# Kernel tuning notes

Measured on AMD Instinct MI355X. Metric: run time of the kernel, lower is better.

The kernel has to match this reference:

```python
import jax, jax.numpy as jnp
import numpy as np

B, S, D, H, L, DFF = 16, 256, 768, 12, 6, 2048
IMG, P, C = 256, 16, 3
HD = D // H
EPS = 1e-5


def _n(k, shp, scale=0.02):
    return jax.random.normal(k, shp, jnp.float32) * scale


def setup_inputs() -> dict:
    key = jax.random.key(0)
    ks = jax.random.split(key, 9)
    return dict(
        encoded_patches=jax.random.normal(ks[0], (B, S, D), jnp.float32),
        W_self_in=_n(ks[1], (L, 3 * D, D)), b_self_in=jnp.zeros((L, 3 * D), jnp.float32),
        W_self_out=_n(ks[2], (L, D, D)), b_self_out=jnp.zeros((L, D), jnp.float32),
        W_cross_in=_n(ks[3], (L, 3 * D, D)), b_cross_in=jnp.zeros((L, 3 * D), jnp.float32),
        W_cross_out=_n(ks[4], (L, D, D)), b_cross_out=jnp.zeros((L, D), jnp.float32),
        ln1_g=jnp.ones((L, D), jnp.float32), ln1_b=jnp.zeros((L, D), jnp.float32),
        ln2_g=jnp.ones((L, D), jnp.float32), ln2_b=jnp.zeros((L, D), jnp.float32),
        ln3_g=jnp.ones((L, D), jnp.float32), ln3_b=jnp.zeros((L, D), jnp.float32),
        W_ff1=_n(ks[5], (L, DFF, D)), b_ff1=jnp.zeros((L, DFF), jnp.float32),
        W_ff2=_n(ks[6], (L, D, DFF)), b_ff2=jnp.zeros((L, D), jnp.float32),
        W_patch=_n(ks[7], (C * P * P, D)), b_patch=jnp.zeros((C * P * P,), jnp.float32),
    )


def sinusoidal_pe(seq, d):
    pos = jnp.arange(seq, dtype=jnp.float32)[:, None]
    div = jnp.exp(jnp.arange(0, d, 2, dtype=jnp.float32) * (-np.log(10000.0) / d))
    pe = jnp.zeros((seq, d), jnp.float32)
    pe = pe.at[:, 0::2].set(jnp.sin(pos * div))
    pe = pe.at[:, 1::2].set(jnp.cos(pos * div))
    return pe


def layer_norm(x, g, b):
    mu = x.mean(-1, keepdims=True)
    var = ((x - mu) ** 2).mean(-1, keepdims=True)
    return (x - mu) * jax.lax.rsqrt(var + EPS) * g + b


def mha(q_in, kv_in, W_in, b_in, W_out, b_out, mask):
    # W_in: [3D, D] packed q,k,v (PyTorch in_proj layout); Linear: y = x W^T + b
    Wq, Wk, Wv = jnp.split(W_in, 3, axis=0)
    bq, bk, bv = jnp.split(b_in, 3, axis=0)
    Bq = q_in.shape[0]
    q = (q_in @ Wq.T + bq).reshape(Bq, -1, H, HD)
    k = (kv_in @ Wk.T + bk).reshape(Bq, -1, H, HD)
    v = (kv_in @ Wv.T + bv).reshape(Bq, -1, H, HD)
    scores = jnp.einsum('bqhd,bkhd->bhqk', q, k) / np.sqrt(HD)
    if mask is not None:
        scores = scores + mask  # mask broadcasts [S, S] with -inf above diag
    attn = jax.nn.softmax(scores, axis=-1)
    out = jnp.einsum('bhqk,bkhd->bqhd', attn, v).reshape(Bq, -1, D)
    return out @ W_out.T + b_out


def reference(encoded_patches, W_self_in, b_self_in, W_self_out, b_self_out,
              W_cross_in, b_cross_in, W_cross_out, b_cross_out,
              ln1_g, ln1_b, ln2_g, ln2_b, ln3_g, ln3_b,
              W_ff1, b_ff1, W_ff2, b_ff2, W_patch, b_patch):
    # The original loops over growing prefixes i=1..S and takes the last
    # position each time. With a causal self-attn mask and per-position
    # cross-attn/FFN/LN, that is mathematically identical to one full
    # causal pass; we compute it once. (eval mode: dropout = identity)
    pe = sinusoidal_pe(S, D)
    causal = jnp.where(jnp.triu(jnp.ones((S, S), jnp.float32), 1) > 0, -jnp.inf, 0.0)
    mem = encoded_patches
    x = encoded_patches + pe[None, :, :]
    for l in range(L):
        # post-norm TransformerDecoderLayer (PyTorch default norm_first=False)
        x = layer_norm(x + mha(x, x, W_self_in[l], b_self_in[l],
                               W_self_out[l], b_self_out[l], causal),
                       ln1_g[l], ln1_b[l])
        x = layer_norm(x + mha(x, mem, W_cross_in[l], b_cross_in[l],
                               W_cross_out[l], b_cross_out[l], None),
                       ln2_g[l], ln2_b[l])
        ff = jax.nn.relu(x @ W_ff1[l].T + b_ff1[l]) @ W_ff2[l].T + b_ff2[l]
        x = layer_norm(x + ff, ln3_g[l], ln3_b[l])
    out = x @ W_patch.T + b_patch                       # [B, S, C*P*P]
    out = out.reshape(-1, IMG, IMG, C)                  # naive view, as in source
    return jnp.transpose(out, (0, 3, 1, 2))             # [B, C, IMG, IMG]
```

## Files before the change

kernel.cpp:

```cpp
#include <hip/hip_runtime.h>
#include <hip/hip_bf16.h>

#define DEV __device__ __forceinline__

typedef __bf16 bf16x8 __attribute__((ext_vector_type(8)));
typedef __bf16 bf16x4 __attribute__((ext_vector_type(4)));
typedef float  f32x4  __attribute__((ext_vector_type(4)));

DEV bf16x8 cvt8(const float4 a, const float4 b) {
    bf16x8 r;
    r[0] = (__bf16)a.x; r[1] = (__bf16)a.y; r[2] = (__bf16)a.z; r[3] = (__bf16)a.w;
    r[4] = (__bf16)b.x; r[5] = (__bf16)b.y; r[6] = (__bf16)b.z; r[7] = (__bf16)b.w;
    return r;
}

DEV void gload_lds16(const __bf16* g, __bf16* l) {
    __builtin_amdgcn_global_load_lds(
        (const __attribute__((address_space(1))) void*)g,
        (__attribute__((address_space(3))) void*)l, 16, 0, 0);
}

DEV int swzcol(int col, int row) {
    return (col & ~63) | ((((col >> 3) & 7) ^ (row & 7)) << 3) | (col & 7);
}

DEV void wconv_one(const float* __restrict__ src, __bf16* __restrict__ dst,
                   int lg, int gpr, int K) {
    const int n = lg / gpr;
    const int gi = lg - n * gpr;
    const int cb = (gi >> 3) << 6;
    const int g = gi & 7;
    const float* sp = src + (size_t)n * K + cb + ((g ^ (n & 7)) << 3);
    float4 a = *(const float4*)sp;
    float4 b = *(const float4*)(sp + 4);
    *(bf16x8*)&dst[(size_t)lg * 8] = cvt8(a, b);
}

__global__ __launch_bounds__(256) void wconv(const float* __restrict__ W,
                                             __bf16* __restrict__ Wb) {
    const int gid = blockIdx.x * 256 + threadIdx.x;
    wconv_one(W, Wb, gid, 96, 768);
}

__global__ __launch_bounds__(256) void wconv4(const float* __restrict__ s0,
                                              const float* __restrict__ s1,
                                              const float* __restrict__ s2,
                                              const float* __restrict__ s3,
                                              __bf16* __restrict__ dst) {
    const int gid = blockIdx.x * 256 + threadIdx.x;
    if (gid < 221184)      wconv_one(s0, dst,           gid,          96, 768);
    else if (gid < 294912) wconv_one(s1, dst + 1769472, gid - 221184, 96, 768);
    else if (gid < 516096) wconv_one(s2, dst + 2359296, gid - 294912, 96, 768);
    else                   wconv_one(s3, dst + 4128768, gid - 516096, 96, 768);
}

__global__ __launch_bounds__(256) void wconv_ff(const float* __restrict__ f1,
                                                const float* __restrict__ f2,
                                                __bf16* __restrict__ dst) {
    const int gid = blockIdx.x * 256 + threadIdx.x;
    if (gid < 196608) wconv_one(f1, dst,           gid,          96, 768);
    else              wconv_one(f2, dst + 1572864, gid - 196608, 256, 2048);
}

template <int RELU, int OUT, int BN>
__global__ __launch_bounds__(256) void gemm_bt(const __bf16* __restrict__ Xb,
                                               const __bf16* __restrict__ Wb,
                                               const float* __restrict__ bias,
                                               float* __restrict__ Yf,
                                               __bf16* __restrict__ Yb,
                                               int ldy, int K) {
    __shared__ __bf16 As[128 * 64];
    __shared__ __bf16 Bs[BN * 64];

    const int tid = threadIdx.x;
    const int lane = tid & 63;
    const int wave = tid >> 6;
    constexpr int NI = (BN == 128) ? 4 : 2;
    const int wr = (BN == 128) ? (wave >> 1) : wave;
    const int wc = (BN == 128) ? (wave & 1) : 0;
    const int lr = lane & 15;

    const int nx = gridDim.x;
    int bid = blockIdx.y * nx + blockIdx.x;
    const int cpx = (nx * gridDim.y) >> 3;
    bid = (bid & 7) * cpx + (bid >> 3);
    const int by = bid / nx;
    const int bx = bid - by * nx;
    const int mBase = by * 128;
    const int nBase = bx * BN;

    const int brow = lane >> 3;
    const __bf16* Ap = Xb + (size_t)mBase * K + ((lane & 7) << 3);
    const __bf16* Bp = Wb + (size_t)nBase * K + ((lane & 7) << 3);

    f32x4 acc[NI][4];
#pragma unroll
    for (int i = 0; i < NI; ++i)
#pragma unroll
        for (int j = 0; j < 4; ++j) {
            f32x4 z = {0.f, 0.f, 0.f, 0.f};
            acc[i][j] = z;
        }

    for (int kt = 0; kt < K; kt += 64) {
#pragma unroll
        for (int i = 0; i < 4; ++i) {
            const int r0 = (wave << 5) + (i << 3);
            gload_lds16(Ap + (size_t)(r0 + brow) * K + kt, &As[r0 << 6]);
        }
#pragma unroll
        for (int i = 0; i < BN / 32; ++i) {
            const int r0 = wave * (BN / 4) + (i << 3);
            gload_lds16(Bp + (size_t)(r0 + brow) * K + kt, &Bs[r0 << 6]);
        }
        __syncthreads();
#pragma unroll
        for (int kk = 0; kk < 2; ++kk) {
            const int q = (lane >> 4) + (kk << 2);
            bf16x8 af[NI], bfv[4];
#pragma unroll
            for (int i = 0; i < NI; ++i) {
                const int r = wr * (NI * 16) + i * 16 + lr;
                af[i] = *(const bf16x8*)&As[(r << 6) + ((q ^ (r & 7)) << 3)];
            }
#pragma unroll
            for (int j = 0; j < 4; ++j) {
                const int r = wc * 64 + j * 16 + lr;
                bfv[j] = *(const bf16x8*)&Bs[(r << 6) + ((q ^ (r & 7)) << 3)];
            }
#pragma unroll
            for (int i = 0; i < NI; ++i)
#pragma unroll
                for (int j = 0; j < 4; ++j)
                    acc[i][j] = __builtin_amdgcn_mfma_f32_16x16x32_bf16(af[i], bfv[j], acc[i][j], 0, 0, 0);
        }
        __syncthreads();
    }

    const int rsub = (lane >> 4) << 2;
#pragma unroll
    for (int i = 0; i < NI; ++i)
#pragma unroll
        for (int j = 0; j < 4; ++j) {
            const int col = nBase + wc * 64 + j * 16 + lr;
            const float bv = bias[col];
#pragma unroll
            for (int rr = 0; rr < 4; ++rr) {
                const int row = mBase + wr * (NI * 16) + i * 16 + rsub + rr;
                float v = acc[i][j][rr] + bv;
                if (RELU) v = fmaxf(v, 0.f);
                if (OUT == 1) {
                    Yb[(size_t)row * ldy + swzcol(col, row)] = (__bf16)v;
                } else if (OUT == 2) {
                    const int b_ = row >> 8, s_ = row & 255;
                    const int w_ = col / 3, c_ = col - w_ * 3;
                    Yf[(size_t)b_ * 196608 + (size_t)c_ * 65536 + s_ * 256 + w_] = v;
                } else {
                    Yf[(size_t)row * ldy + col] = v;
                }
            }
        }
}

__global__ __launch_bounds__(256) void attn_mfma(const __bf16* __restrict__ QKV,
                                                 __bf16* __restrict__ Oout,
                                                 int causal) {
    const int bh = blockIdx.x;
    const int qq = blockIdx.y;
    const int b = bh / 12, h = bh - b * 12;
    const int tid = threadIdx.x;
    const int lane = tid & 63;
    const int w = tid >> 6;
    const int g = lane >> 4;
    const int c = lane & 15;
    const int c7 = c & 7;

    __shared__ __bf16 Ks[64 * 64];
    __shared__ __bf16 Vs[64 * 66];

    const int q64 = (w << 4) + c;
    const int qrow = (qq << 6) + q64;
    const __bf16* qp = QKV + (size_t)((b << 8) + qrow) * 2304 + (h << 6);
    bf16x8 qf0 = *(const bf16x8*)(qp + ((g ^ c7) << 3));
    bf16x8 qf1 = *(const bf16x8*)(qp + (((g + 4) ^ c7) << 3));

    f32x4 oacc[4];
#pragma unroll
    for (int i = 0; i < 4; ++i) { f32x4 z = {0.f, 0.f, 0.f, 0.f}; oacc[i] = z; }
    float mrun = -1e30f, lrun = 0.f;

    const int nt = causal ? (qq + 1) : 4;
    const int sr = tid >> 2;
    const int sg0 = (tid & 3) << 1;
    const int sp = sg0 << 3;

    for (int kt = 0; kt < nt; ++kt) {
        __syncthreads();
        {
            const __bf16* Kp = QKV + (size_t)((b << 8) + (kt << 6)) * 2304 + 768 + (h << 6) + ((lane & 7) << 3);
#pragma unroll
            for (int i = 0; i < 2; ++i) {
                const int r0 = (w << 4) + (i << 3);
                gload_lds16(Kp + (size_t)(r0 + (lane >> 3)) * 2304, &Ks[r0 << 6]);
            }
        }
        {
            const __bf16* vp = QKV + (size_t)((b << 8) + (kt << 6) + sr) * 2304 + 1536 + (h << 6);
            bf16x8 v0 = *(const bf16x8*)(vp + sp);
            bf16x8 v1 = *(const bf16x8*)(vp + sp + 8);
            const int s7 = sr & 7;
            uint32_t* d0 = (uint32_t*)&Vs[sr * 66 + ((sg0 ^ s7) << 3)];
            uint32_t* d1 = (uint32_t*)&Vs[sr * 66 + (((sg0 + 1) ^ s7) << 3)];
            const uint32_t* u0 = (const uint32_t*)&v0;
            const uint32_t* u1 = (const uint32_t*)&v1;
            d0[0] = u0[0]; d0[1] = u0[1]; d0[2] = u0[2]; d0[3] = u0[3];
            d1[0] = u1[0]; d1[1] = u1[1]; d1[2] = u1[2]; d1[3] = u1[3];
        }
        __syncthreads();

        f32x4 sc[4];
#pragma unroll
        for (int mf = 0; mf < 4; ++mf) { f32x4 z = {0.f, 0.f, 0.f, 0.f}; sc[mf] = z; }
#pragma unroll
        for (int mf = 0; mf < 4; ++mf) {
            const int row = (mf << 4) + c;
            bf16x8 af0 = *(const bf16x8*)&Ks[(row << 6) + ((g ^ c7) << 3)];
            sc[mf] = __builtin_amdgcn_mfma_f32_16x16x32_bf16(af0, qf0, sc[mf], 0, 0, 0);
            bf16x8 af1 = *(const bf16x8*)&Ks[(row << 6) + (((g + 4) ^ c7) << 3)];
            sc[mf] = __builtin_amdgcn_mfma_f32_16x16x32_bf16(af1, qf1, sc[mf], 0, 0, 0);
        }

        const int diag = (causal && kt == qq);
        float tm = -1e30f;
#pragma unroll
        for (int mf = 0; mf < 4; ++mf)
#pragma unroll
            for (int r = 0; r < 4; ++r) {
                float v = sc[mf][r] * 0.125f;
                if (diag && ((mf << 4) + (g << 2) + r > q64)) v = -1e30f;
                sc[mf][r] = v;
                tm = fmaxf(tm, v);
            }
        tm = fmaxf(tm, __shfl_xor(tm, 16));
        tm = fmaxf(tm, __shfl_xor(tm, 32));
        const float mnew = fmaxf(mrun, tm);
        const float rs = __expf(mrun - mnew);
        mrun = mnew;
        lrun *= rs;
#pragma unroll
        for (int i = 0; i < 4; ++i) {
            oacc[i][0] *= rs; oacc[i][1] *= rs; oacc[i][2] *= rs; oacc[i][3] *= rs;
        }

        __shared__ __bf16 Ps[64 * 64];
#pragma unroll
        for (int mf = 0; mf < 4; ++mf) {
            const int kg = (mf << 1) + (g >> 1);
            const int e = (g & 1) << 2;
#pragma unroll
            for (int r = 0; r < 4; ++r) {
                float p = __expf(sc[mf][r] - mnew);
                lrun += p;
                Ps[(q64 << 6) + ((kg ^ c7) << 3) + e + r] = (__bf16)p;
            }
        }

#pragma unroll
        for (int kc = 0; kc < 2; ++kc) {
            bf16x8 pb = *(const bf16x8*)&Ps[(q64 << 6) + (((g + (kc << 2)) ^ c7) << 3)];
#pragma unroll
            for (int df = 0; df < 4; ++df) {
                bf16x8 av;
#pragma unroll
                for (int j = 0; j < 8; ++j)
                    av[j] = Vs[((g << 3) + j + (kc << 5)) * 66 + (df << 4) + c];
                oacc[df] = __builtin_amdgcn_mfma_f32_16x16x32_bf16(av, pb, oacc[df], 0, 0, 0);
            }
        }
    }

    lrun += __shfl_xor(lrun, 16);
    lrun += __shfl_xor(lrun, 32);
    const float inv = 1.f / lrun;
    __bf16* op = Oout + (size_t)((b << 8) + qrow) * 768 + (h << 6);
#pragma unroll
    for (int df = 0; df < 4; ++df) {
        bf16x4 ov;
        ov[0] = (__bf16)(oacc[df][0] * inv);
        ov[1] = (__bf16)(oacc[df][1] * inv);
        ov[2] = (__bf16)(oacc[df][2] * inv);
        ov[3] = (__bf16)(oacc[df][3] * inv);
        const int gran = (df << 1) + (g >> 1);
        *(bf16x4*)(op + ((gran ^ c7) << 3) + ((g & 1) << 2)) = ov;
    }
}

__global__ __launch_bounds__(256) void resid_ln(float* __restrict__ x,
                                                __bf16* __restrict__ xb,
                                                const float* __restrict__ r,
                                                const float* __restrict__ g,
                                                const float* __restrict__ b) {
    const int row = blockIdx.x, tid = threadIdx.x;
    float* xp = x + (size_t)row * 768;
    __bf16* xbp = xb + (size_t)row * 768;
    const float* rp = r + (size_t)row * 768;

    float v0 = xp[tid] + rp[tid];
    float v1 = xp[tid + 256] + rp[tid + 256];
    float v2 = xp[tid + 512] + rp[tid + 512];

    __shared__ float red[4];
    float s = v0 + v1 + v2;
#pragma unroll
    for (int off = 32; off > 0; off >>= 1) s += __shfl_down(s, off, 64);
    if ((tid & 63) == 0) red[tid >> 6] = s;
    __syncthreads();
    const float mean = (red[0] + red[1] + red[2] + red[3]) * (1.0f / 768.0f);
    __syncthreads();

    float d0 = v0 - mean, d1 = v1 - mean, d2 = v2 - mean;
    float q = d0 * d0 + d1 * d1 + d2 * d2;
#pragma unroll
    for (int off = 32; off > 0; off >>= 1) q += __shfl_down(q, off, 64);
    if ((tid & 63) == 0) red[tid >> 6] = q;
    __syncthreads();
    const float inv = rsqrtf((red[0] + red[1] + red[2] + red[3]) * (1.0f / 768.0f) + 1e-5f);

    const float o0 = d0 * inv * g[tid] + b[tid];
    const float o1 = d1 * inv * g[tid + 256] + b[tid + 256];
    const float o2 = d2 * inv * g[tid + 512] + b[tid + 512];
    xp[tid] = o0;       xbp[swzcol(tid, row)] = (__bf16)o0;
    xp[tid + 256] = o1; xbp[swzcol(tid + 256, row)] = (__bf16)o1;
    xp[tid + 512] = o2; xbp[swzcol(tid + 512, row)] = (__bf16)o2;
}

__global__ __launch_bounds__(256) void add_pe(const float* __restrict__ e,
                                              float* __restrict__ x,
                                              __bf16* __restrict__ xb,
                                              __bf16* __restrict__ encb) {
    const int gid = blockIdx.x * 256 + threadIdx.x;
    const int m = gid / 96;
    const int g8 = gid - m * 96;
    const int col0 = g8 << 3;
    const int s = m & 255;

    float4 e0 = *(const float4*)(e + (size_t)m * 768 + col0);
    float4 e1 = *(const float4*)(e + (size_t)m * 768 + col0 + 4);

    float pe[8];
#pragma unroll
    for (int p = 0; p < 4; ++p) {
        const int d = col0 + 2 * p;
        const float div = __expf((float)d * (-0.011992630693328381f));
        const float ang = (float)s * div;
        pe[2 * p] = __sinf(ang);
        pe[2 * p + 1] = __cosf(ang);
    }
    float4 v0, v1;
    v0.x = e0.x + pe[0]; v0.y = e0.y + pe[1]; v0.z = e0.z + pe[2]; v0.w = e0.w + pe[3];
    v1.x = e1.x + pe[4]; v1.y = e1.y + pe[5]; v1.z = e1.z + pe[6]; v1.w = e1.w + pe[7];

    *(float4*)(x + (size_t)m * 768 + col0) = v0;
    *(float4*)(x + (size_t)m * 768 + col0 + 4) = v1;

    const int scb = (col0 & ~63) | ((((g8 & 7) ^ (m & 7)) << 3));
    *(bf16x8*)&xb[(size_t)m * 768 + scb] = cvt8(v0, v1);
    *(bf16x8*)&encb[(size_t)m * 768 + scb] = cvt8(e0, e1);
}

extern "C" void kernel_launch(void* const* d_in, const int* in_sizes, int n_in,
                              void* d_out, int out_size, void* d_ws, size_t ws_size,
                              hipStream_t stream) {
    const float* enc         = (const float*)d_in[0];
    const float* W_self_in   = (const float*)d_in[1];
    const float* b_self_in   = (const float*)d_in[2];
    const float* W_self_out  = (const float*)d_in[3];
    const float* b_self_out  = (const float*)d_in[4];
    const float* W_cross_in  = (const float*)d_in[5];
    const float* b_cross_in  = (const float*)d_in[6];
    const float* W_cross_out = (const float*)d_in[7];
    const float* b_cross_out = (const float*)d_in[8];
    const float* ln1_g       = (const float*)d_in[9];
    const float* ln1_b       = (const float*)d_in[10];
    const float* ln2_g       = (const float*)d_in[11];
    const float* ln2_b       = (const float*)d_in[12];
    const float* ln3_g       = (const float*)d_in[13];
    const float* ln3_b       = (const float*)d_in[14];
    const float* W_ff1       = (const float*)d_in[15];
    const float* b_ff1       = (const float*)d_in[16];
    const float* W_ff2       = (const float*)d_in[17];
    const float* b_ff2       = (const float*)d_in[18];
    const float* W_patch     = (const float*)d_in[19];
    const float* b_patch     = (const float*)d_in[20];

    float* out = (float*)d_out;
    float* ws  = (float*)d_ws;

    float*  x       = ws;
    __bf16* xb      = (__bf16*)(ws + 3145728);
    __bf16* qkvb    = (__bf16*)(ws + 4718592);
    __bf16* attnout = (__bf16*)(ws + 9437184);
    float*  proj    = ws + 11010048;
    __bf16* encb    = (__bf16*)(ws + 14155776);
    __bf16* wbuf    = (__bf16*)(ws + 15728640);

    add_pe<<<1536, 256, 0, stream>>>(enc, x, xb, encb);

    for (int l = 0; l < 6; ++l) {
        const float* Wsi = W_self_in   + (size_t)l * 2304 * 768;
        const float* Wso = W_self_out  + (size_t)l * 768 * 768;
        const float* Wci = W_cross_in  + (size_t)l * 2304 * 768;
        const float* Wco = W_cross_out + (size_t)l * 768 * 768;
        const float* Wf1 = W_ff1       + (size_t)l * 2048 * 768;
        const float* Wf2 = W_ff2       + (size_t)l * 768 * 2048;

        wconv4<<<2304, 256, 0, stream>>>(Wsi, Wso, Wci, Wco, wbuf);

        gemm_bt<0, 1, 128><<<dim3(18, 32), 256, 0, stream>>>(xb, wbuf, b_self_in + l * 2304,
                                                             nullptr, qkvb, 2304, 768);
        attn_mfma<<<dim3(192, 4), 256, 0, stream>>>(qkvb, attnout, 1);
        gemm_bt<0, 0, 64><<<dim3(12, 32), 256, 0, stream>>>(attnout, wbuf + 1769472,
                                                            b_self_out + l * 768,
                                                            proj, nullptr, 768, 768);
        resid_ln<<<4096, 256, 0, stream>>>(x, xb, proj, ln1_g + l * 768, ln1_b + l * 768);

        gemm_bt<0, 1, 64><<<dim3(12, 32), 256, 0, stream>>>(xb, wbuf + 2359296,
                                                            b_cross_in + l * 2304,
                                                            nullptr, qkvb, 2304, 768);
        gemm_bt<0, 1, 128><<<dim3(12, 32), 256, 0, stream>>>(encb, wbuf + 2949120,
                                                             b_cross_in + l * 2304 + 768,
                                                             nullptr, qkvb + 768, 2304, 768);
        attn_mfma<<<dim3(192, 4), 256, 0, stream>>>(qkvb, attnout, 0);
        gemm_bt<0, 0, 64><<<dim3(12, 32), 256, 0, stream>>>(attnout, wbuf + 4128768,
                                                            b_cross_out + l * 768,
                                                            proj, nullptr, 768, 768);
        resid_ln<<<4096, 256, 0, stream>>>(x, xb, proj, ln2_g + l * 768, ln2_b + l * 768);

        wconv_ff<<<1536, 256, 0, stream>>>(Wf1, Wf2, wbuf);
        gemm_bt<1, 1, 128><<<dim3(16, 32), 256, 0, stream>>>(xb, wbuf, b_ff1 + l * 2048,
                                                             nullptr, qkvb, 2048, 768);
        gemm_bt<0, 0, 64><<<dim3(12, 32), 256, 0, stream>>>(qkvb, wbuf + 1572864,
                                                            b_ff2 + l * 768,
                                                            proj, nullptr, 768, 2048);
        resid_ln<<<4096, 256, 0, stream>>>(x, xb, proj, ln3_g + l * 768, ln3_b + l * 768);
    }

    wconv<<<288, 256, 0, stream>>>(W_patch, wbuf);
    gemm_bt<0, 2, 64><<<dim3(12, 32), 256, 0, stream>>>(xb, wbuf, b_patch,
                                                        out, nullptr, 768, 768);
}
```

Baseline: 1.450 ms.

## Double-buffer GEMM LDS loads and emit bf16 projection outputs for residual LN

The GEMM main loop now keeps two LDS buffers. It issues the next k-tile's global-to-LDS loads before computing on the current one, using a partial vmcnt wait and raw barriers in place of full __syncthreads, so loads overlap MFMA work. Separately, the output-projection and FF2 GEMMs write bf16 instead of fp32, and resid_ln reads bf16 residuals, which halves that intermediate traffic. The cost is twice the LDS per block, which may lower occupancy, and extra rounding of the residual branch to bf16.

Result: faster. 1.352 ms (-6.7%).

```diff
diff --git a/kernel.cpp b/kernel.cpp
--- a/kernel.cpp
+++ b/kernel.cpp
@@ -2,6 +2,7 @@
 #include <hip/hip_bf16.h>
 
 #define DEV __device__ __forceinline__
+#define WAITVM(N) asm volatile("s_waitcnt vmcnt(" #N ")" ::: "memory")
 
 typedef __bf16 bf16x8 __attribute__((ext_vector_type(8)));
 typedef __bf16 bf16x4 __attribute__((ext_vector_type(4)));
@@ -69,8 +70,10 @@
                                                float* __restrict__ Yf,
                                                __bf16* __restrict__ Yb,
                                                int ldy, int K) {
-    __shared__ __bf16 As[128 * 64];
-    __shared__ __bf16 Bs[BN * 64];
+    constexpr int ABUF = 128 * 64;
+    constexpr int BBUF = BN * 64;
+    __shared__ __bf16 As[2 * ABUF];
+    __shared__ __bf16 Bs[2 * BBUF];
 
     const int tid = threadIdx.x;
     const int lane = tid & 63;
@@ -102,18 +105,20 @@
             acc[i][j] = z;
         }
 
-    for (int kt = 0; kt < K; kt += 64) {
+    auto STAGE = [&](int sel, int kt) {
 #pragma unroll
         for (int i = 0; i < 4; ++i) {
             const int r0 = (wave << 5) + (i << 3);
-            gload_lds16(Ap + (size_t)(r0 + brow) * K + kt, &As[r0 << 6]);
+            gload_lds16(Ap + (size_t)(r0 + brow) * K + kt, &As[sel * ABUF + (r0 << 6)]);
         }
 #pragma unroll
         for (int i = 0; i < BN / 32; ++i) {
             const int r0 = wave * (BN / 4) + (i << 3);
-            gload_lds16(Bp + (size_t)(r0 + brow) * K + kt, &Bs[r0 << 6]);
-        }
-        __syncthreads();
+            gload_lds16(Bp + (size_t)(r0 + brow) * K + kt, &Bs[sel * BBUF + (r0 << 6)]);
+        }
+    };
+
+    auto COMPUTE = [&](int sel) {
 #pragma unroll
         for (int kk = 0; kk < 2; ++kk) {
             const int q = (lane >> 4) + (kk << 2);
@@ -121,12 +126,12 @@
 #pragma unroll
             for (int i = 0; i < NI; ++i) {
                 const int r = wr * (NI * 16) + i * 16 + lr;
-                af[i] = *(const bf16x8*)&As[(r << 6) + ((q ^ (r & 7)) << 3)];
+                af[i] = *(const bf16x8*)&As[sel * ABUF + (r << 6) + ((q ^ (r & 7)) << 3)];
             }
 #pragma unroll
             for (int j = 0; j < 4; ++j) {
                 const int r = wc * 64 + j * 16 + lr;
-                bfv[j] = *(const bf16x8*)&Bs[(r << 6) + ((q ^ (r & 7)) << 3)];
+                bfv[j] = *(const bf16x8*)&Bs[sel * BBUF + (r << 6) + ((q ^ (r & 7)) << 3)];
             }
 #pragma unroll
             for (int i = 0; i < NI; ++i)
@@ -134,8 +139,24 @@
                 for (int j = 0; j < 4; ++j)
                     acc[i][j] = __builtin_amdgcn_mfma_f32_16x16x32_bf16(af[i], bfv[j], acc[i][j], 0, 0, 0);
         }
-        __syncthreads();
+    };
+
+    STAGE(0, 0);
+    int sel = 0;
+    for (int kt = 0; kt + 64 < K; kt += 64) {
+        STAGE(sel ^ 1, kt + 64);
+        if constexpr (BN == 128) WAITVM(8); else WAITVM(6);
+        __builtin_amdgcn_s_barrier();
+        __builtin_amdgcn_sched_barrier(0);
+        COMPUTE(sel);
+        __builtin_amdgcn_sched_barrier(0);
+        __builtin_amdgcn_s_barrier();
+        sel ^= 1;
     }
+    WAITVM(0);
+    __builtin_amdgcn_s_barrier();
+    __builtin_amdgcn_sched_barrier(0);
+    COMPUTE(sel);
 
     const int rsub = (lane >> 4) << 2;
 #pragma unroll
@@ -156,7 +177,7 @@
                     const int w_ = col / 3, c_ = col - w_ * 3;
                     Yf[(size_t)b_ * 196608 + (size_t)c_ * 65536 + s_ * 256 + w_] = v;
                 } else {
-                    Yf[(size_t)row * ldy + col] = v;
+                    Yb[(size_t)row * ldy + col] = (__bf16)v;
                 }
             }
         }
@@ -297,17 +318,17 @@
 
 __global__ __launch_bounds__(256) void resid_ln(float* __restrict__ x,
                                                 __bf16* __restrict__ xb,
-                                                const float* __restrict__ r,
+                                                const __bf16* __restrict__ r,
                                                 const float* __restrict__ g,
                                                 const float* __restrict__ b) {
     const int row = blockIdx.x, tid = threadIdx.x;
     float* xp = x + (size_t)row * 768;
     __bf16* xbp = xb + (size_t)row * 768;
-    const float* rp = r + (size_t)row * 768;
-
-    float v0 = xp[tid] + rp[tid];
-    float v1 = xp[tid + 256] + rp[tid + 256];
-    float v2 = xp[tid + 512] + rp[tid + 512];
+    const __bf16* rp = r + (size_t)row * 768;
+
+    float v0 = xp[tid] + (float)rp[tid];
+    float v1 = xp[tid + 256] + (float)rp[tid + 256];
+    float v2 = xp[tid + 512] + (float)rp[tid + 512];
 
     __shared__ float red[4];
     float s = v0 + v1 + v2;
@@ -400,7 +421,7 @@
     __bf16* xb      = (__bf16*)(ws + 3145728);
     __bf16* qkvb    = (__bf16*)(ws + 4718592);
     __bf16* attnout = (__bf16*)(ws + 9437184);
-    float*  proj    = ws + 11010048;
+    __bf16* projb   = (__bf16*)(ws + 11010048);
     __bf16* encb    = (__bf16*)(ws + 14155776);
     __bf16* wbuf    = (__bf16*)(ws + 15728640);
 
@@ -419,10 +440,10 @@
         gemm_bt<0, 1, 128><<<dim3(18, 32), 256, 0, stream>>>(xb, wbuf, b_self_in + l * 2304,
                                                              nullptr, qkvb, 2304, 768);
         attn_mfma<<<dim3(192, 4), 256, 0, stream>>>(qkvb, attnout, 1);
-        gemm_bt<0, 0, 64><<<dim3(12, 32), 256, 0, stream>>>(attnout, wbuf + 1769472,
+        gemm_bt<0, 3, 64><<<dim3(12, 32), 256, 0, stream>>>(attnout, wbuf + 1769472,
                                                             b_self_out + l * 768,
-                                                            proj, nullptr, 768, 768);
-        resid_ln<<<4096, 256, 0, stream>>>(x, xb, proj, ln1_g + l * 768, ln1_b + l * 768);
+                                                            nullptr, projb, 768, 768);
+        resid_ln<<<4096, 256, 0, stream>>>(x, xb, projb, ln1_g + l * 768, ln1_b + l * 768);
 
         gemm_bt<0, 1, 64><<<dim3(12, 32), 256, 0, stream>>>(xb, wbuf + 2359296,
                                                             b_cross_in + l * 2304,
@@ -431,18 +452,18 @@
                                                              b_cross_in + l * 2304 + 768,
                                                              nullptr, qkvb + 768, 2304, 768);
         attn_mfma<<<dim3(192, 4), 256, 0, stream>>>(qkvb, attnout, 0);
-        gemm_bt<0, 0, 64><<<dim3(12, 32), 256, 0, stream>>>(attnout, wbuf + 4128768,
+        gemm_bt<0, 3, 64><<<dim3(12, 32), 256, 0, stream>>>(attnout, wbuf + 4128768,
                                                             b_cross_out + l * 768,
-                                                            proj, nullptr, 768, 768);
-        resid_ln<<<4096, 256, 0, stream>>>(x, xb, proj, ln2_g + l * 768, ln2_b + l * 768);
+                                                            nullptr, projb, 768, 768);
+        resid_ln<<<4096, 256, 0, stream>>>(x, xb, projb, ln2_g + l * 768, ln2_b + l * 768);
 
         wconv_ff<<<1536, 256, 0, stream>>>(Wf1, Wf2, wbuf);
         gemm_bt<1, 1, 128><<<dim3(16, 32), 256, 0, stream>>>(xb, wbuf, b_ff1 + l * 2048,
                                                              nullptr, qkvb, 2048, 768);
-        gemm_bt<0, 0, 64><<<dim3(12, 32), 256, 0, stream>>>(qkvb, wbuf + 1572864,
+        gemm_bt<0, 3, 64><<<dim3(12, 32), 256, 0, stream>>>(qkvb, wbuf + 1572864,
                                                             b_ff2 + l * 768,
-                                                            proj, nullptr, 768, 2048);
-        resid_ln<<<4096, 256, 0, stream>>>(x, xb, proj, ln3_g + l * 768, ln3_b + l * 768);
+                                                            nullptr, projb, 768, 2048);
+        resid_ln<<<4096, 256, 0, stream>>>(x, xb, projb, ln3_g + l * 768, ln3_b + l * 768);
     }
 
     wconv<<<288, 256, 0, stream>>>(W_patch, wbuf);
```
